# Performance work log

Measured on AMD Instinct MI355X. Metric: run time of the kernel, lower is better.

The kernel has to match this reference:

```python
import jax, jax.numpy as jnp
import numpy as np

N, E, C, EC, L, G = 100000, 1600000, 128, 16, 3, 256
GN_EPS = 1e-5


def setup_inputs() -> dict:
    key = jax.random.key(0)
    ks = jax.random.split(key, 16)
    inp = {}
    inp["x"] = jax.random.normal(ks[0], (N, C), dtype=jnp.float32)
    inp["edge_attr"] = jax.random.normal(ks[1], (E, EC), dtype=jnp.float32)
    inp["edge_index"] = jax.random.randint(ks[2], (2, E), 0, N, dtype=jnp.int64)
    inp["batch"] = jnp.sort(jax.random.randint(ks[3], (N,), 0, G, dtype=jnp.int64))
    # lin_edge: Linear(EC, C) + silu
    inp["lin_edge_w"] = jax.random.normal(ks[4], (EC, C), dtype=jnp.float32) / np.sqrt(EC)
    inp["lin_edge_b"] = jnp.zeros((C,), dtype=jnp.float32)
    # per-layer GINEConv MLP: Linear(C,C) -> silu -> Linear(C,C)
    s = 1.0 / np.sqrt(C)
    inp["conv_w1"] = jax.random.normal(ks[5], (L, C, C), dtype=jnp.float32) * s
    inp["conv_b1"] = jnp.zeros((L, C), dtype=jnp.float32)
    inp["conv_w2"] = jax.random.normal(ks[6], (L, C, C), dtype=jnp.float32) * s
    inp["conv_b2"] = jnp.zeros((L, C), dtype=jnp.float32)
    # per-layer GraphNorm params (weight=1, bias=0, mean_scale=1 at init)
    inp["gn_weight"] = jnp.ones((L, C), dtype=jnp.float32)
    inp["gn_bias"] = jnp.zeros((L, C), dtype=jnp.float32)
    inp["gn_mean_scale"] = jnp.ones((L, C), dtype=jnp.float32)
    return inp


def reference(x, edge_attr, edge_index, batch, lin_edge_w, lin_edge_b,
              conv_w1, conv_b1, conv_w2, conv_b2,
              gn_weight, gn_bias, gn_mean_scale):
    src, dst = edge_index[0], edge_index[1]
    # lin_edge: project raw edge features to channel dim
    e = jax.nn.silu(edge_attr @ lin_edge_w + lin_edge_b)  # [E, C]
    # per-graph node counts for GraphNorm means
    cnt = jax.ops.segment_sum(jnp.ones((N, 1), x.dtype), batch, num_segments=G)  # [G,1]
    for l in range(L):
        # GINEConv: relu(x_j + e), scatter-sum to target, (1+eps)*x + aggr, eps=0
        msg = jax.nn.relu(x[src] + e)                                  # [E, C]
        aggr = jax.ops.segment_sum(msg, dst, num_segments=N)           # [N, C]
        h = x + aggr
        h = jax.nn.silu(h @ conv_w1[l] + conv_b1[l]) @ conv_w2[l] + conv_b2[l]
        # GraphNorm: per-graph mean/var with learnable mean_scale
        mean = jax.ops.segment_sum(h, batch, num_segments=G) / cnt     # [G, C]
        out = h - mean[batch] * gn_mean_scale[l]
        var = jax.ops.segment_sum(out * out, batch, num_segments=G) / cnt
        std = jnp.sqrt(var + GN_EPS)
        x = gn_weight[l] * out / std[batch] + gn_bias[l]
    return x
```

## Files before the change

### kernel.cpp

```cpp
#include <hip/hip_runtime.h>
#include <hip/hip_fp16.h>

#define N_NODES 100000
#define N_EDGES 1600000
#define C_DIM 128
#define EC_DIM 16
#define L_LAYERS 3
#define G_GRAPHS 256
#define GN_EPS 1e-5f
#define SCAN_BLOCKS 391

__device__ __forceinline__ float silu_f(float v) {
    return v / (1.0f + __expf(-v));
}

__device__ __forceinline__ float4 ld4(const float* p) { return *(const float4*)p; }
__device__ __forceinline__ void st4(float* p, float4 v) { *(float4*)p = v; }
__device__ __forceinline__ float4 fma4(float s, float4 w, float4 a) {
    a.x = fmaf(s, w.x, a.x); a.y = fmaf(s, w.y, a.y);
    a.z = fmaf(s, w.z, a.z); a.w = fmaf(s, w.w, a.w);
    return a;
}


__global__ void zero_cnt_kernel(int* cnt) { cnt[threadIdx.x] = 0; }

__global__ void count_kernel(const int* __restrict__ batch, int* __restrict__ cnt) {
    int i = blockIdx.x * blockDim.x + threadIdx.x;
    if (i < N_NODES) atomicAdd(&cnt[batch[i]], 1);
}

__global__ void scan_kernel(const int* __restrict__ cnt, int* __restrict__ start,
                            float* __restrict__ cntf) {
    __shared__ int s[G_GRAPHS];
    int t = threadIdx.x;
    int v = cnt[t];
    s[t] = v;
    __syncthreads();
    for (int off = 1; off < G_GRAPHS; off <<= 1) {
        int add = (t >= off) ? s[t - off] : 0;
        __syncthreads();
        s[t] += add;
        __syncthreads();
    }
    start[t] = s[t] - v;
    cntf[t] = (float)v;
}


__global__ void deg_count_kernel(const int* __restrict__ eidx, int* __restrict__ deg) {
    int e = blockIdx.x * blockDim.x + threadIdx.x;
    if (e < N_EDGES) atomicAdd(&deg[eidx[N_EDGES + e]], 1);
}

__global__ void scanA_kernel(const int* __restrict__ deg, int* __restrict__ rpl,
                             int* __restrict__ bsum) {
    __shared__ int s[256];
    int i = blockIdx.x * 256 + threadIdx.x;
    int v = (i < N_NODES) ? deg[i] : 0;
    s[threadIdx.x] = v;
    __syncthreads();
    for (int off = 1; off < 256; off <<= 1) {
        int add = (threadIdx.x >= off) ? s[threadIdx.x - off] : 0;
        __syncthreads();
        s[threadIdx.x] += add;
        __syncthreads();
    }
    if (i < N_NODES) rpl[i] = s[threadIdx.x] - v;
    if (threadIdx.x == 255) bsum[blockIdx.x] = s[255];
}

__global__ void scanB_kernel(const int* __restrict__ bsum, int* __restrict__ boff) {
    __shared__ int s[512];
    int t = threadIdx.x;
    int v = (t < SCAN_BLOCKS) ? bsum[t] : 0;
    s[t] = v;
    __syncthreads();
    for (int off = 1; off < 512; off <<= 1) {
        int add = (t >= off) ? s[t - off] : 0;
        __syncthreads();
        s[t] += add;
        __syncthreads();
    }
    if (t < SCAN_BLOCKS) boff[t] = s[t] - v;
}

__global__ void scanC_kernel(const int* __restrict__ rpl, const int* __restrict__ boff,
                             int* __restrict__ rp, int* __restrict__ cursor) {
    int i = blockIdx.x * 256 + threadIdx.x;
    if (i < N_NODES) {
        int v = rpl[i] + boff[blockIdx.x];
        rp[i] = v;
        cursor[i] = v;
    }
    if (i == 0) rp[N_NODES] = N_EDGES;
}

__global__ void fill_kernel(const int* __restrict__ eidx, int* __restrict__ cursor,
                            int* __restrict__ srcs, int* __restrict__ eid) {
    int e = blockIdx.x * blockDim.x + threadIdx.x;
    if (e >= N_EDGES) return;
    int src = eidx[e];
    int dst = eidx[N_EDGES + e];
    int pos = atomicAdd(&cursor[dst], 1);
    srcs[pos] = src;
    eid[pos] = e;
}

__global__ __launch_bounds__(256) void eacopy_kernel(
    const float* __restrict__ ea, const int* __restrict__ eid,
    float4* __restrict__ eac)
{
    long long t = (long long)blockIdx.x * blockDim.x + threadIdx.x;
    int pos = (int)(t >> 2), q = (int)(t & 3);
    if (pos >= N_EDGES) return;
    int e = eid[pos];
    eac[(size_t)pos * 4 + q] = ((const float4*)(ea + (size_t)e * EC_DIM))[q];
}

__global__ __launch_bounds__(256) void xcast_kernel(
    const float* __restrict__ x, __half2* __restrict__ xh)
{
    int i = blockIdx.x * blockDim.x + threadIdx.x;
    if (i < N_NODES * C_DIM / 2) {
        float2 v = ((const float2*)x)[i];
        xh[i] = __floats2half2_rn(v.x, v.y);
    }
}


#define DECLW(k) const float2 w##k = *(const float2*)(Wp + (k) * C_DIM);

#define EDGE_PROJ(QA, QB, QC, QD, ZX, ZY) \
    ZX = b2.x; ZY = b2.y; \
    ZX = fmaf(QA.x, w0.x,  ZX); ZY = fmaf(QA.x, w0.y,  ZY); \
    ZX = fmaf(QA.y, w1.x,  ZX); ZY = fmaf(QA.y, w1.y,  ZY); \
    ZX = fmaf(QA.z, w2.x,  ZX); ZY = fmaf(QA.z, w2.y,  ZY); \
    ZX = fmaf(QA.w, w3.x,  ZX); ZY = fmaf(QA.w, w3.y,  ZY); \
    ZX = fmaf(QB.x, w4.x,  ZX); ZY = fmaf(QB.x, w4.y,  ZY); \
    ZX = fmaf(QB.y, w5.x,  ZX); ZY = fmaf(QB.y, w5.y,  ZY); \
    ZX = fmaf(QB.z, w6.x,  ZX); ZY = fmaf(QB.z, w6.y,  ZY); \
    ZX = fmaf(QB.w, w7.x,  ZX); ZY = fmaf(QB.w, w7.y,  ZY); \
    ZX = fmaf(QC.x, w8.x,  ZX); ZY = fmaf(QC.x, w8.y,  ZY); \
    ZX = fmaf(QC.y, w9.x,  ZX); ZY = fmaf(QC.y, w9.y,  ZY); \
    ZX = fmaf(QC.z, w10.x, ZX); ZY = fmaf(QC.z, w10.y, ZY); \
    ZX = fmaf(QC.w, w11.x, ZX); ZY = fmaf(QC.w, w11.y, ZY); \
    ZX = fmaf(QD.x, w12.x, ZX); ZY = fmaf(QD.x, w12.y, ZY); \
    ZX = fmaf(QD.y, w13.x, ZX); ZY = fmaf(QD.y, w13.y, ZY); \
    ZX = fmaf(QD.z, w14.x, ZX); ZY = fmaf(QD.z, w14.y, ZY); \
    ZX = fmaf(QD.w, w15.x, ZX); ZY = fmaf(QD.w, w15.y, ZY);

template<bool BIG>
__global__ __launch_bounds__(256) void gatherf_kernel(
    const float* __restrict__ x, const __half* __restrict__ xh,
    const float* __restrict__ ea, const float* __restrict__ eac,
    const int* __restrict__ srcs, const int* __restrict__ eid,
    const int* __restrict__ rp,
    const float* __restrict__ W, const float* __restrict__ bias,
    float* __restrict__ hb)
{
    int n = (blockIdx.x * blockDim.x + threadIdx.x) >> 6;
    n = __builtin_amdgcn_readfirstlane(n);
    if (n >= N_NODES) return;
    const int lane = threadIdx.x & 63;
    const int c2 = lane * 2;
    const float* Wp = W + c2;
    DECLW(0)  DECLW(1)  DECLW(2)  DECLW(3)
    DECLW(4)  DECLW(5)  DECLW(6)  DECLW(7)
    DECLW(8)  DECLW(9)  DECLW(10) DECLW(11)
    DECLW(12) DECLW(13) DECLW(14) DECLW(15)
    const float2 b2 = *(const float2*)(bias + c2);

    float accx = 0.f, accy = 0.f;
    const int beg = rp[n], end = rp[n + 1];
    for (int j = beg; j < end; ++j) {
        const int src = srcs[j];
        float4 A0, A1, A2, A3;
        float xsx, xsy;
        if (BIG) {
            const float* ep = eac + (size_t)j * EC_DIM;
            A0 = ld4(ep);     A1 = ld4(ep + 4);
            A2 = ld4(ep + 8); A3 = ld4(ep + 12);
            const __half2 xv = *(const __half2*)(xh + (size_t)src * C_DIM + c2);
            const float2 xf = __half22float2(xv);
            xsx = xf.x; xsy = xf.y;
        } else {
            const int e = eid[j];
            const float* ep = ea + (size_t)e * EC_DIM;
            A0 = ld4(ep);     A1 = ld4(ep + 4);
            A2 = ld4(ep + 8); A3 = ld4(ep + 12);
            const float2 xf = *(const float2*)(x + (size_t)src * C_DIM + c2);
            xsx = xf.x; xsy = xf.y;
        }
        float zx, zy;
        EDGE_PROJ(A0, A1, A2, A3, zx, zy)
        accx += fmaxf(xsx + silu_f(zx), 0.f);
        accy += fmaxf(xsy + silu_f(zy), 0.f);
    }
    const float2 xo = *(const float2*)(x + (size_t)n * C_DIM + c2);
    *(float2*)(hb + (size_t)n * C_DIM + c2) = make_float2(xo.x + accx, xo.y + accy);
}

template<bool SILU>
__global__ __launch_bounds__(256) void gemm128_kernel(
    const float* __restrict__ A, const float* __restrict__ W,
    const float* __restrict__ bias, float* __restrict__ out)
{
    __shared__ float Wl[C_DIM * C_DIM];
    const int tid = threadIdx.x;
    const int rowbase = blockIdx.x * 32;
#pragma unroll
    for (int i = 0; i < 16; ++i)
        ((float4*)Wl)[i * 256 + tid] = ((const float4*)W)[i * 256 + tid];
    __syncthreads();

    const int cx = tid & 31;
    const int ry = tid >> 5;
    const float4 bias4 = ld4(bias + cx * 4);
    float4 acc[4] = {bias4, bias4, bias4, bias4};
    const float* Ab = A + (size_t)(rowbase + ry * 4) * C_DIM;

    for (int k = 0; k < C_DIM; k += 4) {
        float4 a[4], w[4];
#pragma unroll
        for (int rr = 0; rr < 4; ++rr) a[rr] = ld4(Ab + rr * C_DIM + k);
#pragma unroll
        for (int kk = 0; kk < 4; ++kk) w[kk] = *(const float4*)&Wl[(k + kk) * C_DIM + cx * 4];
#pragma unroll
        for (int rr = 0; rr < 4; ++rr) {
            acc[rr] = fma4(a[rr].x, w[0], acc[rr]);
            acc[rr] = fma4(a[rr].y, w[1], acc[rr]);
            acc[rr] = fma4(a[rr].z, w[2], acc[rr]);
            acc[rr] = fma4(a[rr].w, w[3], acc[rr]);
        }
    }
#pragma unroll
    for (int rr = 0; rr < 4; ++rr) {
        float4 v = acc[rr];
        if (SILU) { v.x = silu_f(v.x); v.y = silu_f(v.y); v.z = silu_f(v.z); v.w = silu_f(v.w); }
        st4(out + (size_t)(rowbase + ry * 4 + rr) * C_DIM + cx * 4, v);
    }
}

__global__ __launch_bounds__(1024) void gn_reduce_kernel(
    const float* __restrict__ h, const int* __restrict__ start,
    const int* __restrict__ cnt, const float* __restrict__ cntf,
    const float* __restrict__ ms, float* __restrict__ meansc,
    float* __restrict__ rstd)
{
    const int g = blockIdx.x;
    const int c = threadIdx.x & 127;
    const int sub = threadIdx.x >> 7;
    const int s0 = start[g];
    const int n = cnt[g];
    float sum = 0.f, sq = 0.f;
    for (int r = sub; r < n; r += 8) {
        float v = h[(size_t)(s0 + r) * C_DIM + c];
        sum += v; sq += v * v;
    }
    __shared__ float ls[1024], lq[1024];
    ls[threadIdx.x] = sum; lq[threadIdx.x] = sq;
    __syncthreads();
    if (threadIdx.x < 512) {
        ls[threadIdx.x] += ls[threadIdx.x + 512];
        lq[threadIdx.x] += lq[threadIdx.x + 512];
    }
    __syncthreads();
    if (threadIdx.x < 256) {
        ls[threadIdx.x] += ls[threadIdx.x + 256];
        lq[threadIdx.x] += lq[threadIdx.x + 256];
    }
    __syncthreads();
    if (threadIdx.x < 128) {
        sum = ls[threadIdx.x] + ls[threadIdx.x + 128];
        sq  = lq[threadIdx.x] + lq[threadIdx.x + 128];
        const float cn = cntf[g];
        const float mean = sum / cn;
        const float msq = sq / cn;
        const float s = ms[c];
        const float var = msq - (2.0f * s - s * s) * mean * mean;
        meansc[(size_t)g * C_DIM + c] = mean * s;
        rstd[(size_t)g * C_DIM + c] = 1.0f / sqrtf(var + GN_EPS);
    }
}

__global__ __launch_bounds__(256) void gn_norm_kernel(
    const float* __restrict__ h, const int* __restrict__ batch,
    const float* __restrict__ meansc, const float* __restrict__ rstd,
    const float* __restrict__ gw, const float* __restrict__ gb,
    float* __restrict__ out, __half* __restrict__ xh, int wxh)
{
    const int id = blockIdx.x * blockDim.x + threadIdx.x;
    const int row = id >> 5;
    const int c4 = (id & 31) * 4;
    if (row >= N_NODES) return;
    const int g = batch[row];
    const float4 hv = ld4(h + (size_t)row * C_DIM + c4);
    const float4 m = ld4(meansc + (size_t)g * C_DIM + c4);
    const float4 r = ld4(rstd + (size_t)g * C_DIM + c4);
    const float4 w = ld4(gw + c4);
    const float4 b = ld4(gb + c4);
    float4 o;
    o.x = fmaf((hv.x - m.x) * r.x, w.x, b.x);
    o.y = fmaf((hv.y - m.y) * r.y, w.y, b.y);
    o.z = fmaf((hv.z - m.z) * r.z, w.z, b.z);
    o.w = fmaf((hv.w - m.w) * r.w, w.w, b.w);
    st4(out + (size_t)row * C_DIM + c4, o);
    if (wxh) {
        __half2* xp = (__half2*)(xh + (size_t)row * C_DIM + c4);
        xp[0] = __floats2half2_rn(o.x, o.y);
        xp[1] = __floats2half2_rn(o.z, o.w);
    }
}


extern "C" void kernel_launch(void* const* d_in, const int* in_sizes, int n_in,
                              void* d_out, int out_size, void* d_ws, size_t ws_size,
                              hipStream_t stream)
{
    const float* x_in      = (const float*)d_in[0];
    const float* edge_attr = (const float*)d_in[1];
    const int*   edge_idx  = (const int*)d_in[2];
    const int*   batch     = (const int*)d_in[3];
    const float* lew       = (const float*)d_in[4];
    const float* leb       = (const float*)d_in[5];
    const float* w1        = (const float*)d_in[6];
    const float* b1        = (const float*)d_in[7];
    const float* w2        = (const float*)d_in[8];
    const float* b2        = (const float*)d_in[9];
    const float* gnw       = (const float*)d_in[10];
    const float* gnb       = (const float*)d_in[11];
    const float* gms       = (const float*)d_in[12];
    float* out = (float*)d_out;

    float* hbuf   = (float*)d_ws;
    float* meansc = hbuf + (size_t)N_NODES * C_DIM;
    float* rstd   = meansc + (size_t)G_GRAPHS * C_DIM;
    float* cntf   = rstd + (size_t)G_GRAPHS * C_DIM;
    int*   cnti   = (int*)(cntf + G_GRAPHS);
    int*   startg = cnti + G_GRAPHS;
    int*   deg    = startg + G_GRAPHS;
    int*   rpl    = deg + N_NODES;
    int*   bsum   = rpl + N_NODES;
    int*   boff   = bsum + 512;
    int*   rp     = boff + 512;
    int*   cursor = rp + N_NODES + 2;
    int*   srcs   = cursor + N_NODES;
    int*   eid    = srcs + N_EDGES;
    float* eac    = (float*)(eid + N_EDGES);
    __half* xh    = (__half*)(eac + (size_t)N_EDGES * EC_DIM);

    const size_t need_big = (size_t)((char*)(xh + (size_t)N_NODES * C_DIM) - (char*)d_ws);
    const bool big = ws_size >= need_big;

    zero_cnt_kernel<<<1, G_GRAPHS, 0, stream>>>(cnti);
    count_kernel<<<(N_NODES + 255) / 256, 256, 0, stream>>>(batch, cnti);
    scan_kernel<<<1, G_GRAPHS, 0, stream>>>(cnti, startg, cntf);

    hipMemsetAsync(deg, 0, (size_t)N_NODES * sizeof(int), stream);
    deg_count_kernel<<<(N_EDGES + 255) / 256, 256, 0, stream>>>(edge_idx, deg);
    scanA_kernel<<<SCAN_BLOCKS, 256, 0, stream>>>(deg, rpl, bsum);
    scanB_kernel<<<1, 512, 0, stream>>>(bsum, boff);
    scanC_kernel<<<SCAN_BLOCKS, 256, 0, stream>>>(rpl, boff, rp, cursor);
    fill_kernel<<<(N_EDGES + 255) / 256, 256, 0, stream>>>(edge_idx, cursor, srcs, eid);

    if (big) {
        eacopy_kernel<<<(int)(((size_t)N_EDGES * 4 + 255) / 256), 256, 0, stream>>>(
            edge_attr, eid, (float4*)eac);
        xcast_kernel<<<(int)(((size_t)N_NODES * C_DIM / 2 + 255) / 256), 256, 0, stream>>>(
            x_in, (__half2*)xh);
    }

    const float* cur = x_in;
    for (int l = 0; l < L_LAYERS; ++l) {
        if (big) {
            gatherf_kernel<true><<<(int)(((size_t)N_NODES * 64 + 255) / 256), 256, 0, stream>>>(
                cur, xh, edge_attr, eac, srcs, eid, rp, lew, leb, hbuf);
        } else {
            gatherf_kernel<false><<<(int)(((size_t)N_NODES * 64 + 255) / 256), 256, 0, stream>>>(
                cur, xh, edge_attr, eac, srcs, eid, rp, lew, leb, hbuf);
        }
        gemm128_kernel<true><<<N_NODES / 32, 256, 0, stream>>>(
            hbuf, w1 + (size_t)l * C_DIM * C_DIM, b1 + (size_t)l * C_DIM, out);
        gemm128_kernel<false><<<N_NODES / 32, 256, 0, stream>>>(
            out, w2 + (size_t)l * C_DIM * C_DIM, b2 + (size_t)l * C_DIM, hbuf);
        gn_reduce_kernel<<<G_GRAPHS, 1024, 0, stream>>>(
            hbuf, startg, cnti, cntf, gms + (size_t)l * C_DIM, meansc, rstd);
        gn_norm_kernel<<<(int)(((size_t)N_NODES * 32 + 255) / 256), 256, 0, stream>>>(
            hbuf, batch, meansc, rstd, gnw + (size_t)l * C_DIM, gnb + (size_t)l * C_DIM,
            out, xh, (big && l < L_LAYERS - 1) ? 1 : 0);
        cur = out;
    }
}
```

Before: 1.727 ms.

## Run node MLP GEMMs on fp16 MFMA with half-precision intermediates

Adds an MFMA-based 128x128 GEMM kernel (16x16x32 f16) that replaces the FP32 shared-memory GEMMs on the big-workspace path. The gather kernel now writes its result in fp16, the first GEMM writes its SiLU output in fp16, and the weights are transposed and cast to fp16 once up front. The aim is to cut GEMM arithmetic cost and the memory traffic of the intermediates. The gather kernel also gets a launch-bounds occupancy hint, and the workspace is re-laid out with 256-byte aligned allocations. The cost is lower precision in the hidden activations, and the fast path now needs a larger workspace.

```diff
diff --git a/kernel.cpp b/kernel.cpp
--- a/kernel.cpp
+++ b/kernel.cpp
@@ -9,6 +9,9 @@
 #define G_GRAPHS 256
 #define GN_EPS 1e-5f
 #define SCAN_BLOCKS 391
+
+typedef __attribute__((ext_vector_type(8))) _Float16 f16x8;
+typedef __attribute__((ext_vector_type(4))) float f32x4;
 
 __device__ __forceinline__ float silu_f(float v) {
     return v / (1.0f + __expf(-v));
@@ -126,6 +129,16 @@
         float2 v = ((const float2*)x)[i];
         xh[i] = __floats2half2_rn(v.x, v.y);
     }
+}
+
+__global__ __launch_bounds__(256) void wtcast_kernel(
+    const float* __restrict__ W, __half* __restrict__ Wt)
+{
+    int l = blockIdx.y;
+    int t = blockIdx.x * 256 + threadIdx.x;
+    int c = t >> 7, k = t & 127;
+    Wt[(size_t)l * 16384 + (size_t)c * 128 + k] =
+        __float2half_rn(W[(size_t)l * 16384 + (size_t)k * 128 + c]);
 }
 
 
@@ -151,13 +164,13 @@
     ZX = fmaf(QD.w, w15.x, ZX); ZY = fmaf(QD.w, w15.y, ZY);
 
 template<bool BIG>
-__global__ __launch_bounds__(256) void gatherf_kernel(
+__global__ __launch_bounds__(256, 2) void gatherf_kernel(
     const float* __restrict__ x, const __half* __restrict__ xh,
     const float* __restrict__ ea, const float* __restrict__ eac,
     const int* __restrict__ srcs, const int* __restrict__ eid,
     const int* __restrict__ rp,
     const float* __restrict__ W, const float* __restrict__ bias,
-    float* __restrict__ hb)
+    float* __restrict__ hb, __half* __restrict__ hb16)
 {
     int n = (blockIdx.x * blockDim.x + threadIdx.x) >> 6;
     n = __builtin_amdgcn_readfirstlane(n);
@@ -198,7 +211,62 @@
         accy += fmaxf(xsy + silu_f(zy), 0.f);
     }
     const float2 xo = *(const float2*)(x + (size_t)n * C_DIM + c2);
-    *(float2*)(hb + (size_t)n * C_DIM + c2) = make_float2(xo.x + accx, xo.y + accy);
+    if (BIG) {
+        *(__half2*)(hb16 + (size_t)n * C_DIM + c2) =
+            __floats2half2_rn(xo.x + accx, xo.y + accy);
+    } else {
+        *(float2*)(hb + (size_t)n * C_DIM + c2) = make_float2(xo.x + accx, xo.y + accy);
+    }
+}
+
+template<bool SILU, bool OUT16>
+__global__ __launch_bounds__(256) void gemm_mfma_kernel(
+    const __half* __restrict__ A16, const __half* __restrict__ Wt,
+    const float* __restrict__ bias, float* __restrict__ outf,
+    __half* __restrict__ out16)
+{
+    const int wid  = threadIdx.x >> 6;
+    const int lane = threadIdx.x & 63;
+    const int r16  = lane & 15;
+    const int kq   = lane >> 4;
+    const int rowbase = blockIdx.x * 64 + wid * 16;
+
+    f32x4 acc[8];
+#pragma unroll
+    for (int nt = 0; nt < 8; ++nt) {
+        float bv = bias[nt * 16 + r16];
+        acc[nt] = (f32x4){bv, bv, bv, bv};
+    }
+
+    int arow = rowbase + r16;
+    if (arow >= N_NODES) arow = N_NODES - 1;
+    const __half* Ar = A16 + (size_t)arow * C_DIM + kq * 8;
+    const __half* Br = Wt + (size_t)r16 * C_DIM + kq * 8;
+
+#pragma unroll
+    for (int kt = 0; kt < 4; ++kt) {
+        const f16x8 af = *(const f16x8*)(Ar + kt * 32);
+#pragma unroll
+        for (int nt = 0; nt < 8; ++nt) {
+            const f16x8 bf = *(const f16x8*)(Br + (size_t)nt * 16 * C_DIM + kt * 32);
+            acc[nt] = __builtin_amdgcn_mfma_f32_16x16x32_f16(af, bf, acc[nt], 0, 0, 0);
+        }
+    }
+
+#pragma unroll
+    for (int nt = 0; nt < 8; ++nt) {
+#pragma unroll
+        for (int j = 0; j < 4; ++j) {
+            float v = acc[nt][j];
+            if (SILU) v = silu_f(v);
+            const int m = rowbase + kq * 4 + j;
+            const int nc = nt * 16 + r16;
+            if (m < N_NODES) {
+                if (OUT16) out16[(size_t)m * C_DIM + nc] = __float2half_rn(v);
+                else       outf[(size_t)m * C_DIM + nc] = v;
+            }
+        }
+    }
 }
 
 template<bool SILU>
@@ -333,24 +401,34 @@
     const float* gms       = (const float*)d_in[12];
     float* out = (float*)d_out;
 
-    float* hbuf   = (float*)d_ws;
-    float* meansc = hbuf + (size_t)N_NODES * C_DIM;
-    float* rstd   = meansc + (size_t)G_GRAPHS * C_DIM;
-    float* cntf   = rstd + (size_t)G_GRAPHS * C_DIM;
-    int*   cnti   = (int*)(cntf + G_GRAPHS);
-    int*   startg = cnti + G_GRAPHS;
-    int*   deg    = startg + G_GRAPHS;
-    int*   rpl    = deg + N_NODES;
-    int*   bsum   = rpl + N_NODES;
-    int*   boff   = bsum + 512;
-    int*   rp     = boff + 512;
-    int*   cursor = rp + N_NODES + 2;
-    int*   srcs   = cursor + N_NODES;
-    int*   eid    = srcs + N_EDGES;
-    float* eac    = (float*)(eid + N_EDGES);
-    __half* xh    = (__half*)(eac + (size_t)N_EDGES * EC_DIM);
-
-    const size_t need_big = (size_t)((char*)(xh + (size_t)N_NODES * C_DIM) - (char*)d_ws);
+    char* base = (char*)d_ws;
+    size_t off = 0;
+    auto alloc = [&](size_t bytes) -> void* {
+        void* p = base + off;
+        off = (off + bytes + 255) & ~(size_t)255;
+        return p;
+    };
+    float* hbuf   = (float*)alloc((size_t)N_NODES * C_DIM * 4);
+    float* meansc = (float*)alloc((size_t)G_GRAPHS * C_DIM * 4);
+    float* rstd   = (float*)alloc((size_t)G_GRAPHS * C_DIM * 4);
+    float* cntf   = (float*)alloc(G_GRAPHS * 4);
+    int*   cnti   = (int*)alloc(G_GRAPHS * 4);
+    int*   startg = (int*)alloc(G_GRAPHS * 4);
+    int*   deg    = (int*)alloc((size_t)N_NODES * 4);
+    int*   rpl    = (int*)alloc((size_t)N_NODES * 4);
+    int*   bsum   = (int*)alloc(512 * 4);
+    int*   boff   = (int*)alloc(512 * 4);
+    int*   rp     = (int*)alloc(((size_t)N_NODES + 2) * 4);
+    int*   cursor = (int*)alloc((size_t)N_NODES * 4);
+    int*   srcs   = (int*)alloc((size_t)N_EDGES * 4);
+    int*   eid    = (int*)alloc((size_t)N_EDGES * 4);
+    float* eac    = (float*)alloc((size_t)N_EDGES * EC_DIM * 4);
+    __half* xh    = (__half*)alloc((size_t)N_NODES * C_DIM * 2);
+    __half* hb16  = (__half*)alloc((size_t)N_NODES * C_DIM * 2);
+    __half* t16   = (__half*)alloc((size_t)N_NODES * C_DIM * 2);
+    __half* wt6   = (__half*)alloc((size_t)6 * 16384 * 2);
+
+    const size_t need_big = off;
     const bool big = ws_size >= need_big;
 
     zero_cnt_kernel<<<1, G_GRAPHS, 0, stream>>>(cnti);
@@ -369,21 +447,27 @@
             edge_attr, eid, (float4*)eac);
         xcast_kernel<<<(int)(((size_t)N_NODES * C_DIM / 2 + 255) / 256), 256, 0, stream>>>(
             x_in, (__half2*)xh);
+        wtcast_kernel<<<dim3(64, 3), 256, 0, stream>>>(w1, wt6);
+        wtcast_kernel<<<dim3(64, 3), 256, 0, stream>>>(w2, wt6 + 3 * 16384);
     }
 
     const float* cur = x_in;
     for (int l = 0; l < L_LAYERS; ++l) {
         if (big) {
             gatherf_kernel<true><<<(int)(((size_t)N_NODES * 64 + 255) / 256), 256, 0, stream>>>(
-                cur, xh, edge_attr, eac, srcs, eid, rp, lew, leb, hbuf);
+                cur, xh, edge_attr, eac, srcs, eid, rp, lew, leb, hbuf, hb16);
+            gemm_mfma_kernel<true, true><<<(N_NODES + 63) / 64, 256, 0, stream>>>(
+                hb16, wt6 + (size_t)l * 16384, b1 + (size_t)l * C_DIM, hbuf, t16);
+            gemm_mfma_kernel<false, false><<<(N_NODES + 63) / 64, 256, 0, stream>>>(
+                t16, wt6 + (size_t)(3 + l) * 16384, b2 + (size_t)l * C_DIM, hbuf, t16);
         } else {
             gatherf_kernel<false><<<(int)(((size_t)N_NODES * 64 + 255) / 256), 256, 0, stream>>>(
-                cur, xh, edge_attr, eac, srcs, eid, rp, lew, leb, hbuf);
+                cur, xh, edge_attr, eac, srcs, eid, rp, lew, leb, hbuf, hb16);
+            gemm128_kernel<true><<<N_NODES / 32, 256, 0, stream>>>(
+                hbuf, w1 + (size_t)l * C_DIM * C_DIM, b1 + (size_t)l * C_DIM, out);
+            gemm128_kernel<false><<<N_NODES / 32, 256, 0, stream>>>(
+                out, w2 + (size_t)l * C_DIM * C_DIM, b2 + (size_t)l * C_DIM, hbuf);
         }
-        gemm128_kernel<true><<<N_NODES / 32, 256, 0, stream>>>(
-            hbuf, w1 + (size_t)l * C_DIM * C_DIM, b1 + (size_t)l * C_DIM, out);
-        gemm128_kernel<false><<<N_NODES / 32, 256, 0, stream>>>(
-            out, w2 + (size_t)l * C_DIM * C_DIM, b2 + (size_t)l * C_DIM, hbuf);
         gn_reduce_kernel<<<G_GRAPHS, 1024, 0, stream>>>(
             hbuf, startg, cnti, cntf, gms + (size_t)l * C_DIM, meansc, rstd);
         gn_norm_kernel<<<(int)(((size_t)N_NODES * 32 + 255) / 256), 256, 0, stream>>>(
```

Result: faster. 1.534 ms (-11.2%).
